# Kernel optimization log

Hardware: AMD Instinct MI355X
Metric: run time of the kernel (lower is better)

## Reference

```python
import jax, jax.numpy as jnp
import numpy as np

B, C, H, W = 8, 32, 512, 512
WS = 8
CQ = C // 4                      # 8
N = (H // WS) * (W // WS)        # 4096 windows
ED = WS * WS * C                 # 2048 embed_dim
EPS = 1e-6


def setup_inputs() -> dict:
    key = jax.random.key(0)
    ks = jax.random.split(key, 16)
    s = 0.02
    return {
        "input_x": jax.random.normal(ks[0], (B, C, H, W), jnp.float32),
        # in_conv: Conv2d(C, C//4, 1)
        "w_in": jax.random.normal(ks[1], (CQ, C), jnp.float32) * s,
        "b_in": jnp.zeros((CQ,), jnp.float32),
        # conv: Conv2d(C, C//4, 1) + LayerNorm(C//4)
        "w_conv": jax.random.normal(ks[2], (CQ, C), jnp.float32) * s,
        "b_conv": jnp.zeros((CQ,), jnp.float32),
        "ln_w": jnp.ones((CQ,), jnp.float32),
        "ln_b": jnp.zeros((CQ,), jnp.float32),
        # out_CA: Conv2d(C//4, C, 1)
        "w_ca": jax.random.normal(ks[3], (C, CQ), jnp.float32) * s,
        "b_ca": jnp.zeros((C,), jnp.float32),
        # out_SA: Conv2d(C//4, 1, 3, pad 1)
        "w_sa": jax.random.normal(ks[4], (1, CQ, 3, 3), jnp.float32) * s,
        "b_sa": jnp.zeros((1,), jnp.float32),
        # out_mask MLP: Linear(ED, ED//2), Linear(ED//2, ED)  (torch weight [out,in])
        "w_m1": jax.random.normal(ks[5], (ED // 2, ED), jnp.float32) * s,
        "b_m1": jnp.zeros((ED // 2,), jnp.float32),
        "w_m2": jax.random.normal(ks[6], (ED, ED // 2), jnp.float32) * s,
        "b_m2": jnp.zeros((ED,), jnp.float32),
    }


def _leaky(x):
    return jax.nn.leaky_relu(x, 0.1)


def _conv1x1(x, w, b):
    # x: [B,Cin,H,W], w: [Cout,Cin]
    return jnp.einsum('bchw,oc->bohw', x, w) + b[None, :, None, None]


def reference(input_x, w_in, b_in, w_conv, b_conv, ln_w, ln_b,
              w_ca, b_ca, w_sa, b_sa, w_m1, b_m1, w_m2, b_m2):
    b_, c_, h_, w_ = input_x.shape
    n_win = (h_ // WS) * (w_ // WS)

    # in_conv branch
    x = _leaky(_conv1x1(input_x, w_in, b_in))          # [B,CQ,H,W]

    # conv branch: 1x1 conv -> channels_first LayerNorm -> leaky
    x_ = _conv1x1(input_x, w_conv, b_conv)             # [B,CQ,H,W]
    u = jnp.mean(x_, axis=1, keepdims=True)
    s = jnp.mean((x_ - u) ** 2, axis=1, keepdims=True)
    x_ = (x_ - u) / jnp.sqrt(s + EPS)
    x_ = _leaky(ln_w[None, :, None, None] * x_ + ln_b[None, :, None, None])

    # channel attention: global avg pool -> 1x1 conv -> sigmoid
    pooled = jnp.mean(x_, axis=(2, 3), keepdims=True)  # [B,CQ,1,1]
    ca = jax.nn.sigmoid(_conv1x1(pooled, w_ca, b_ca))  # [B,C,1,1]

    # spatial attention: 3x3 conv -> sigmoid
    sa = jax.lax.conv_general_dilated(
        x_, w_sa, (1, 1), 'SAME',
        dimension_numbers=('NCHW', 'OIHW', 'NCHW')) + b_sa[None, :, None, None]
    sa = jax.nn.sigmoid(sa)                            # [B,1,H,W]

    # window variance + bottom-k mask
    xm = jnp.mean(x, axis=1)                           # [B,H,W]
    xw = xm.reshape(b_, h_ // WS, WS, w_ // WS, WS)
    xw = xw.transpose(0, 1, 3, 2, 4).reshape(b_, n_win, WS * WS)  # [B,N,64]
    var_x = jnp.var(xw, axis=-1, ddof=1)               # [B,N] (torch unbiased var)
    k_top = n_win // 2
    _, idx = jax.lax.top_k(-var_x, k_top)              # indices of smallest-variance windows
    mask = jnp.ones((b_, n_win), input_x.dtype)
    mask = mask.at[jnp.arange(b_)[:, None], idx].set(0.0)  # vectorized scatter

    # broadcast 0/1 mask across embed dim, then MLP (see notes re: original bug)
    m = jnp.broadcast_to(mask[:, :, None], (b_, n_win, w_m1.shape[1]))
    hdd = _leaky(jnp.einsum('bnd,ed->bne', m, w_m1) + b_m1)
    out_mask = jnp.einsum('bne,fe->bnf', hdd, w_m2) + b_m2  # [B,N,ED]

    return (out_mask, ca, sa)
```

## Files before the change

kernel.cpp:

```cpp
#include <hip/hip_runtime.h>
#include <math.h>

#define B_   8
#define C_   32
#define H_   512
#define W_   512
#define CQ_  8
#define NW_  4096
#define ED_  2048
#define EH_  1024
#define EPS_ 1e-6f

#define TW 64
#define TH 16
#define XLH 18
#define XLW 68

__device__ __forceinline__ float leaky(float x) { return x > 0.f ? x : 0.1f * x; }
__device__ __forceinline__ float sigmoidf_(float x) { return 1.f / (1.f + __expf(-x)); }

__global__ __launch_bounds__(256, 3) void pass_a(
    const float* __restrict__ x,
    const float* __restrict__ w_in, const float* __restrict__ b_in,
    const float* __restrict__ w_conv, const float* __restrict__ b_conv,
    const float* __restrict__ ln_w, const float* __restrict__ ln_b,
    const float* __restrict__ w_sa, const float* __restrict__ b_sa,
    float* __restrict__ sa_out, double* __restrict__ var_out,
    float* __restrict__ pooled_part)
{
    __shared__ float xl[CQ_][XLH][XLW];
    __shared__ float xm_lds[TH][TW];
    __shared__ float red[4][CQ_];

    const int tid = threadIdx.x;
    const int b  = blockIdx.z;
    const int ty = blockIdx.y * TH, tx = blockIdx.x * TW;
    const int px = (tid & 15) * 4, py = tid >> 4;
    const size_t plane = (size_t)H_ * W_;
    const float* xb = x + (size_t)b * C_ * plane;
    const float* p  = xb + (size_t)(ty + py) * W_ + (tx + px);

    int hy = 0, hx = 1;
    if (tid < 66)        { hy = 0;         hx = tid + 1; }
    else if (tid < 132)  { hy = 17;        hx = tid - 65; }
    else if (tid < 148)  { hy = tid - 131; hx = 1; }
    else if (tid < 164)  { hy = tid - 147; hx = 66; }
    const int gy = ty + hy - 1, gx = tx + hx - 2;
    const bool inb = (tid < 164) && (gy >= 0) && (gy < H_) && (gx >= 0) && (gx < W_);
    const float* ph = inb ? (xb + (size_t)gy * W_ + gx) : xb;

    float ycv[CQ_][4], yin[CQ_][4], hacc[CQ_];
#pragma unroll
    for (int q = 0; q < CQ_; ++q) {
        hacc[q] = 0.f;
#pragma unroll
        for (int j = 0; j < 4; ++j) { ycv[q][j] = 0.f; yin[q][j] = 0.f; }
    }

    float4 ib[2][4];
    float  hb[2][4];
#pragma unroll
    for (int k = 0; k < 4; ++k) {
        ib[0][k] = *reinterpret_cast<const float4*>(p + (size_t)k * plane);
        hb[0][k] = ph[(size_t)k * plane];
    }

#pragma unroll
    for (int cb = 0; cb < 8; ++cb) {
        const int cur = cb & 1;
        if (cb < 7) {
#pragma unroll
            for (int k = 0; k < 4; ++k) {
                const int c = (cb + 1) * 4 + k;
                ib[cur ^ 1][k] = *reinterpret_cast<const float4*>(p + (size_t)c * plane);
                hb[cur ^ 1][k] = ph[(size_t)c * plane];
            }
        }
#pragma unroll
        for (int k = 0; k < 4; ++k) {
            const int c = cb * 4 + k;
            const float4 v = ib[cur][k];
            const float hv = hb[cur][k];
#pragma unroll
            for (int q = 0; q < CQ_; ++q) {
                const float wc = w_conv[q * C_ + c];
                const float wi = w_in[q * C_ + c];
                ycv[q][0] = fmaf(wc, v.x, ycv[q][0]);
                ycv[q][1] = fmaf(wc, v.y, ycv[q][1]);
                ycv[q][2] = fmaf(wc, v.z, ycv[q][2]);
                ycv[q][3] = fmaf(wc, v.w, ycv[q][3]);
                yin[q][0] = fmaf(wi, v.x, yin[q][0]);
                yin[q][1] = fmaf(wi, v.y, yin[q][1]);
                yin[q][2] = fmaf(wi, v.z, yin[q][2]);
                yin[q][3] = fmaf(wi, v.w, yin[q][3]);
                hacc[q]   = fmaf(wc, hv, hacc[q]);
            }
        }
    }

#pragma unroll
    for (int q = 0; q < CQ_; ++q) {
        const float bc = b_conv[q];
#pragma unroll
        for (int j = 0; j < 4; ++j) ycv[q][j] += bc;
    }

    float ps[CQ_];
#pragma unroll
    for (int q = 0; q < CQ_; ++q) ps[q] = 0.f;

    float xmv[4];
#pragma unroll
    for (int j = 0; j < 4; ++j) {
        float u = 0.f;
#pragma unroll
        for (int q = 0; q < CQ_; ++q) u += ycv[q][j];
        u *= 0.125f;
        float s = 0.f;
#pragma unroll
        for (int q = 0; q < CQ_; ++q) { const float d = ycv[q][j] - u; s = fmaf(d, d, s); }
        s *= 0.125f;
        const float inv = 1.f / sqrtf(s + EPS_);
        float m = 0.f;
#pragma unroll
        for (int q = 0; q < CQ_; ++q) {
            const float xv = leaky(fmaf(ln_w[q], (ycv[q][j] - u) * inv, ln_b[q]));
            ycv[q][j] = xv;
            ps[q] += xv;
            m += leaky(yin[q][j] + b_in[q]);
        }
        xmv[j] = m * 0.125f;
    }

    *reinterpret_cast<float4*>(&xm_lds[py][px]) = make_float4(xmv[0], xmv[1], xmv[2], xmv[3]);
#pragma unroll
    for (int q = 0; q < CQ_; ++q) {
        *reinterpret_cast<float2*>(&xl[q][py + 1][px + 2]) = make_float2(ycv[q][0], ycv[q][1]);
        *reinterpret_cast<float2*>(&xl[q][py + 1][px + 4]) = make_float2(ycv[q][2], ycv[q][3]);
    }

    const int lane = tid & 63, wave = tid >> 6;
#pragma unroll
    for (int q = 0; q < CQ_; ++q) {
        float s = ps[q];
#pragma unroll
        for (int off = 32; off; off >>= 1) s += __shfl_xor(s, off);
        if (lane == 0) red[wave][q] = s;
    }

    if (tid < 164) {
        float yc[CQ_];
        float u = 0.f;
#pragma unroll
        for (int q = 0; q < CQ_; ++q) { yc[q] = hacc[q] + b_conv[q]; u += yc[q]; }
        u *= 0.125f;
        float s = 0.f;
#pragma unroll
        for (int q = 0; q < CQ_; ++q) { const float d = yc[q] - u; s = fmaf(d, d, s); }
        s *= 0.125f;
        const float inv = 1.f / sqrtf(s + EPS_);
#pragma unroll
        for (int q = 0; q < CQ_; ++q) {
            const float v = leaky(fmaf(ln_w[q], (yc[q] - u) * inv, ln_b[q]));
            xl[q][hy][hx] = inb ? v : 0.f;
        }
    }

    __syncthreads();

    if (tid < CQ_) {
        const float s = red[0][tid] + red[1][tid] + red[2][tid] + red[3][tid];
        const int bid = (blockIdx.z * gridDim.y + blockIdx.y) * gridDim.x + blockIdx.x;
        pooled_part[bid * CQ_ + tid] = s;
    }

    {
        const float bsa = b_sa[0];
        float acc[4] = {bsa, bsa, bsa, bsa};
#pragma unroll
        for (int q = 0; q < CQ_; ++q) {
#pragma unroll
            for (int dy = 0; dy < 3; ++dy) {
                const float* r = &xl[q][py + dy][px];
                const float4 aa = *reinterpret_cast<const float4*>(r);
                const float4 bb = *reinterpret_cast<const float4*>(r + 4);
                const float v[8] = {aa.x, aa.y, aa.z, aa.w, bb.x, bb.y, bb.z, bb.w};
#pragma unroll
                for (int dx = 0; dx < 3; ++dx) {
                    const float w = w_sa[q * 9 + dy * 3 + dx];
#pragma unroll
                    for (int j = 0; j < 4; ++j) acc[j] = fmaf(w, v[j + dx + 1], acc[j]);
                }
            }
        }
        const float4 o = make_float4(sigmoidf_(acc[0]), sigmoidf_(acc[1]),
                                     sigmoidf_(acc[2]), sigmoidf_(acc[3]));
        *reinterpret_cast<float4*>(&sa_out[((size_t)b * H_ + (ty + py)) * W_ + tx + px]) = o;
    }

#pragma unroll
    for (int k = 0; k < 4; ++k) {
        const int wi = wave * 4 + k;
        const int wy = wi >> 3, wx = wi & 7;
        const double dv = (double)xm_lds[wy * 8 + (lane >> 3)][wx * 8 + (lane & 7)];
        double s = dv;
#pragma unroll
        for (int off = 32; off; off >>= 1) s += __shfl_xor(s, off);
        const double mean = s * (1.0 / 64.0);
        const double d = dv - mean;
        double s2 = d * d;
#pragma unroll
        for (int off = 32; off; off >>= 1) s2 += __shfl_xor(s2, off);
        if (lane == 0) {
            const int n = (blockIdx.y * 2 + wy) * 64 + blockIdx.x * 8 + wx;
            var_out[(size_t)b * NW_ + n] = s2 * (1.0 / 63.0);
        }
    }
}

__global__ __launch_bounds__(256) void k2_kernel(
    const double* __restrict__ var, float* __restrict__ maskF,
    const float* __restrict__ w_m1, const float* __restrict__ b_m1,
    float* __restrict__ h1, float* __restrict__ h0,
    const float* __restrict__ pooled_part,
    const float* __restrict__ w_ca, const float* __restrict__ b_ca,
    float* __restrict__ ca_out)
{
    __shared__ double sv[NW_];
    const int bi = blockIdx.x;
    const int tid = threadIdx.x;

    if (bi < 128) {
        const int b = bi >> 4;
        const double* vb = var + (size_t)b * NW_;
        for (int j = tid; j < NW_; j += 256) sv[j] = vb[j];
        __syncthreads();
        const int i = (bi & 15) * 256 + tid;
        const double vi = sv[i];
        int cnt = 0;
#pragma unroll 4
        for (int j = 0; j < NW_; ++j) {
            const double vj = sv[j];
            cnt += (vj < vi) || (vj == vi && j < i);
        }
        maskF[(size_t)b * NW_ + i] = (cnt < NW_ / 2) ? 0.f : 1.f;
    } else if (bi < 384) {
        const int wave = tid >> 6, lane = tid & 63;
        const int e = (bi - 128) * 4 + wave;
        const float* row = w_m1 + (size_t)e * ED_;
        float s = 0.f;
#pragma unroll
        for (int k = 0; k < ED_ / 64; ++k) s += row[lane + 64 * k];
#pragma unroll
        for (int off = 32; off; off >>= 1) s += __shfl_xor(s, off);
        if (lane == 0) {
            h1[e] = leaky(s + b_m1[e]);
            h0[e] = leaky(b_m1[e]);
        }
    } else {
        float* sp = (float*)sv;
        const int bq = tid >> 2, part = tid & 3;
        const int bb = bq >> 3, q = bq & 7;
        float s = 0.f;
        for (int k = part; k < 256; k += 4) s += pooled_part[((size_t)bb * 256 + k) * CQ_ + q];
        sp[tid] = s;
        __syncthreads();
        if (tid < 64)
            sp[256 + tid] = (sp[4 * tid] + sp[4 * tid + 1] + sp[4 * tid + 2] + sp[4 * tid + 3])
                            * (1.f / ((float)H_ * (float)W_));
        __syncthreads();
        const int ob = tid >> 5, o = tid & 31;
        float acc = b_ca[o];
#pragma unroll
        for (int qq = 0; qq < CQ_; ++qq)
            acc = fmaf(w_ca[o * CQ_ + qq], sp[256 + ob * CQ_ + qq], acc);
        ca_out[tid] = sigmoidf_(acc);
    }
}

__global__ __launch_bounds__(256) void o_kernel(const float* __restrict__ w_m2,
                                                const float* __restrict__ b_m2,
                                                const float* __restrict__ h1,
                                                const float* __restrict__ h0,
                                                float* __restrict__ o1, float* __restrict__ o0)
{
    const int wave = threadIdx.x >> 6, lane = threadIdx.x & 63;
    const int f = blockIdx.x * 4 + wave;
    const float* row = w_m2 + (size_t)f * EH_;
    float s1 = 0.f, s0 = 0.f;
#pragma unroll
    for (int k = 0; k < EH_ / 64; ++k) {
        const float w = row[lane + 64 * k];
        s1 = fmaf(w, h1[lane + 64 * k], s1);
        s0 = fmaf(w, h0[lane + 64 * k], s0);
    }
#pragma unroll
    for (int off = 32; off; off >>= 1) {
        s1 += __shfl_xor(s1, off);
        s0 += __shfl_xor(s0, off);
    }
    if (lane == 0) {
        o1[f] = s1 + b_m2[f];
        o0[f] = s0 + b_m2[f];
    }
}

__global__ __launch_bounds__(256) void bcast_kernel(const float* __restrict__ maskF,
                                                    const float* __restrict__ o1,
                                                    const float* __restrict__ o0,
                                                    float* __restrict__ out)
{
    __shared__ float sm[16];
    const int t = threadIdx.x;
    const long row0 = (long)blockIdx.x * 16;
    if (t < 16) sm[t] = maskF[row0 + t];
    const float4 a1 = ((const float4*)o1)[t], b1 = ((const float4*)o1)[t + 256];
    const float4 a0 = ((const float4*)o0)[t], b0 = ((const float4*)o0)[t + 256];
    __syncthreads();
#pragma unroll
    for (int r = 0; r < 16; ++r) {
        float4* dst = (float4*)(out + (size_t)(row0 + r) * ED_);
        const bool m = sm[r] > 0.5f;
        dst[t]       = m ? a1 : a0;
        dst[t + 256] = m ? b1 : b0;
    }
}

extern "C" void kernel_launch(void* const* d_in, const int* in_sizes, int n_in,
                              void* d_out, int out_size, void* d_ws, size_t ws_size,
                              hipStream_t stream)
{
    const float* x    = (const float*)d_in[0];
    const float* w_in = (const float*)d_in[1];
    const float* b_in = (const float*)d_in[2];
    const float* w_cv = (const float*)d_in[3];
    const float* b_cv = (const float*)d_in[4];
    const float* lnw  = (const float*)d_in[5];
    const float* lnb  = (const float*)d_in[6];
    const float* w_ca = (const float*)d_in[7];
    const float* b_ca = (const float*)d_in[8];
    const float* w_sa = (const float*)d_in[9];
    const float* b_sa = (const float*)d_in[10];
    const float* w_m1 = (const float*)d_in[11];
    const float* b_m1 = (const float*)d_in[12];
    const float* w_m2 = (const float*)d_in[13];
    const float* b_m2 = (const float*)d_in[14];

    float* out_mask = (float*)d_out;
    float* ca_out   = out_mask + (size_t)B_ * NW_ * ED_;
    float* sa_out   = ca_out + (size_t)B_ * C_;

    char* ws = (char*)d_ws;
    double* var       = (double*)ws;
    float*  maskF     = (float*)(ws + (size_t)B_ * NW_ * 8);
    float*  pooled_pp = maskF + (size_t)B_ * NW_;
    float*  h1 = pooled_pp + 2048 * CQ_;
    float*  h0 = h1 + EH_;
    float*  o1 = h0 + EH_;
    float*  o0 = o1 + ED_;

    pass_a<<<dim3(W_ / TW, H_ / TH, B_), 256, 0, stream>>>(
        x, w_in, b_in, w_cv, b_cv, lnw, lnb, w_sa, b_sa, sa_out, var, pooled_pp);
    k2_kernel<<<385, 256, 0, stream>>>(var, maskF, w_m1, b_m1, h1, h0,
                                       pooled_pp, w_ca, b_ca, ca_out);
    o_kernel<<<ED_ / 4, 256, 0, stream>>>(w_m2, b_m2, h1, h0, o1, o0);
    bcast_kernel<<<B_ * NW_ / 16, 256, 0, stream>>>(maskF, o1, o0, out_mask);
}
```

Before: 331.8 us.

## Split spatial-attention conv into separate kernel and stage input via global_load_lds

The first pass no longer recomputes the LayerNorm branch on a 1-pixel halo for the 3x3 conv. Instead it writes the normalized CQ-channel map into the (later overwritten) out_mask buffer, and a new sa_kernel does the 3x3 conv plus sigmoid from that intermediate. The input channel loads are moved to asynchronous global-to-LDS copies, double-buffered and synchronized with barriers, and the occupancy hint is raised from 3 to 4. This removes the halo loads and redundant halo compute in exchange for an extra 64MB write and read of the intermediate and an additional kernel launch.

```diff
diff --git a/kernel.cpp b/kernel.cpp
--- a/kernel.cpp
+++ b/kernel.cpp
@@ -13,22 +13,23 @@
 
 #define TW 64
 #define TH 16
-#define XLH 18
-#define XLW 68
+
+#define AS1 __attribute__((address_space(1)))
+#define AS3 __attribute__((address_space(3)))
 
 __device__ __forceinline__ float leaky(float x) { return x > 0.f ? x : 0.1f * x; }
 __device__ __forceinline__ float sigmoidf_(float x) { return 1.f / (1.f + __expf(-x)); }
 
-__global__ __launch_bounds__(256, 3) void pass_a(
+__global__ __launch_bounds__(256, 4) void pass_a(
     const float* __restrict__ x,
     const float* __restrict__ w_in, const float* __restrict__ b_in,
     const float* __restrict__ w_conv, const float* __restrict__ b_conv,
     const float* __restrict__ ln_w, const float* __restrict__ ln_b,
-    const float* __restrict__ w_sa, const float* __restrict__ b_sa,
-    float* __restrict__ sa_out, double* __restrict__ var_out,
+    float* __restrict__ xq_out,
+    double* __restrict__ var_out,
     float* __restrict__ pooled_part)
 {
-    __shared__ float xl[CQ_][XLH][XLW];
+    __shared__ float stage[2][4][TH][TW];
     __shared__ float xm_lds[TH][TW];
     __shared__ float red[4][CQ_];
 
@@ -36,51 +37,49 @@
     const int b  = blockIdx.z;
     const int ty = blockIdx.y * TH, tx = blockIdx.x * TW;
     const int px = (tid & 15) * 4, py = tid >> 4;
+    const int lane = tid & 63, wv = tid >> 6;
     const size_t plane = (size_t)H_ * W_;
     const float* xb = x + (size_t)b * C_ * plane;
-    const float* p  = xb + (size_t)(ty + py) * W_ + (tx + px);
-
-    int hy = 0, hx = 1;
-    if (tid < 66)        { hy = 0;         hx = tid + 1; }
-    else if (tid < 132)  { hy = 17;        hx = tid - 65; }
-    else if (tid < 148)  { hy = tid - 131; hx = 1; }
-    else if (tid < 164)  { hy = tid - 147; hx = 66; }
-    const int gy = ty + hy - 1, gx = tx + hx - 2;
-    const bool inb = (tid < 164) && (gy >= 0) && (gy < H_) && (gx >= 0) && (gx < W_);
-    const float* ph = inb ? (xb + (size_t)gy * W_ + gx) : xb;
-
-    float ycv[CQ_][4], yin[CQ_][4], hacc[CQ_];
-#pragma unroll
-    for (int q = 0; q < CQ_; ++q) {
-        hacc[q] = 0.f;
+
+    const float* gsrc[4];
+#pragma unroll
+    for (int i = 0; i < 4; ++i) {
+        const int j = i * 64 + lane;
+        const int r = j >> 4, c4 = j & 15;
+        gsrc[i] = xb + (size_t)wv * plane + (size_t)(ty + r) * W_ + tx + c4 * 4;
+    }
+
+#define STAGE(bufidx, cb)                                                     \
+    {                                                                         \
+        _Pragma("unroll")                                                     \
+        for (int i_ = 0; i_ < 4; ++i_) {                                      \
+            __builtin_amdgcn_global_load_lds(                                 \
+                (const AS1 unsigned int*)(gsrc[i_] + (size_t)(cb) * 4 * plane),\
+                (AS3 unsigned int*)(&stage[bufidx][wv][0][0] + i_ * 256),     \
+                16, 0, 0);                                                    \
+        }                                                                     \
+    }
+
+    float ycv[CQ_][4], yin[CQ_][4];
+#pragma unroll
+    for (int q = 0; q < CQ_; ++q)
 #pragma unroll
         for (int j = 0; j < 4; ++j) { ycv[q][j] = 0.f; yin[q][j] = 0.f; }
-    }
-
-    float4 ib[2][4];
-    float  hb[2][4];
-#pragma unroll
-    for (int k = 0; k < 4; ++k) {
-        ib[0][k] = *reinterpret_cast<const float4*>(p + (size_t)k * plane);
-        hb[0][k] = ph[(size_t)k * plane];
-    }
-
+
+    STAGE(0, 0);
 #pragma unroll
     for (int cb = 0; cb < 8; ++cb) {
-        const int cur = cb & 1;
         if (cb < 7) {
-#pragma unroll
-            for (int k = 0; k < 4; ++k) {
-                const int c = (cb + 1) * 4 + k;
-                ib[cur ^ 1][k] = *reinterpret_cast<const float4*>(p + (size_t)c * plane);
-                hb[cur ^ 1][k] = ph[(size_t)c * plane];
-            }
-        }
+            STAGE((cb + 1) & 1, cb + 1);
+            asm volatile("s_waitcnt vmcnt(4)" ::: "memory");
+        } else {
+            asm volatile("s_waitcnt vmcnt(0)" ::: "memory");
+        }
+        asm volatile("s_barrier" ::: "memory");
 #pragma unroll
         for (int k = 0; k < 4; ++k) {
             const int c = cb * 4 + k;
-            const float4 v = ib[cur][k];
-            const float hv = hb[cur][k];
+            const float4 v = *reinterpret_cast<const float4*>(&stage[cb & 1][k][py][px]);
 #pragma unroll
             for (int q = 0; q < CQ_; ++q) {
                 const float wc = w_conv[q * C_ + c];
@@ -93,10 +92,11 @@
                 yin[q][1] = fmaf(wi, v.y, yin[q][1]);
                 yin[q][2] = fmaf(wi, v.z, yin[q][2]);
                 yin[q][3] = fmaf(wi, v.w, yin[q][3]);
-                hacc[q]   = fmaf(wc, hv, hacc[q]);
             }
         }
-    }
+        asm volatile("s_barrier" ::: "memory");
+    }
+#undef STAGE
 
 #pragma unroll
     for (int q = 0; q < CQ_; ++q) {
@@ -132,38 +132,21 @@
         xmv[j] = m * 0.125f;
     }
 
+#pragma unroll
+    for (int q = 0; q < CQ_; ++q) {
+        *reinterpret_cast<float4*>(
+            &xq_out[(((size_t)b * CQ_ + q) * H_ + (ty + py)) * W_ + tx + px]) =
+            make_float4(ycv[q][0], ycv[q][1], ycv[q][2], ycv[q][3]);
+    }
+
     *reinterpret_cast<float4*>(&xm_lds[py][px]) = make_float4(xmv[0], xmv[1], xmv[2], xmv[3]);
-#pragma unroll
-    for (int q = 0; q < CQ_; ++q) {
-        *reinterpret_cast<float2*>(&xl[q][py + 1][px + 2]) = make_float2(ycv[q][0], ycv[q][1]);
-        *reinterpret_cast<float2*>(&xl[q][py + 1][px + 4]) = make_float2(ycv[q][2], ycv[q][3]);
-    }
-
-    const int lane = tid & 63, wave = tid >> 6;
+
 #pragma unroll
     for (int q = 0; q < CQ_; ++q) {
         float s = ps[q];
 #pragma unroll
         for (int off = 32; off; off >>= 1) s += __shfl_xor(s, off);
-        if (lane == 0) red[wave][q] = s;
-    }
-
-    if (tid < 164) {
-        float yc[CQ_];
-        float u = 0.f;
-#pragma unroll
-        for (int q = 0; q < CQ_; ++q) { yc[q] = hacc[q] + b_conv[q]; u += yc[q]; }
-        u *= 0.125f;
-        float s = 0.f;
-#pragma unroll
-        for (int q = 0; q < CQ_; ++q) { const float d = yc[q] - u; s = fmaf(d, d, s); }
-        s *= 0.125f;
-        const float inv = 1.f / sqrtf(s + EPS_);
-#pragma unroll
-        for (int q = 0; q < CQ_; ++q) {
-            const float v = leaky(fmaf(ln_w[q], (yc[q] - u) * inv, ln_b[q]));
-            xl[q][hy][hx] = inb ? v : 0.f;
-        }
+        if (lane == 0) red[wv][q] = s;
     }
 
     __syncthreads();
@@ -174,33 +157,9 @@
         pooled_part[bid * CQ_ + tid] = s;
     }
 
-    {
-        const float bsa = b_sa[0];
-        float acc[4] = {bsa, bsa, bsa, bsa};
-#pragma unroll
-        for (int q = 0; q < CQ_; ++q) {
-#pragma unroll
-            for (int dy = 0; dy < 3; ++dy) {
-                const float* r = &xl[q][py + dy][px];
-                const float4 aa = *reinterpret_cast<const float4*>(r);
-                const float4 bb = *reinterpret_cast<const float4*>(r + 4);
-                const float v[8] = {aa.x, aa.y, aa.z, aa.w, bb.x, bb.y, bb.z, bb.w};
-#pragma unroll
-                for (int dx = 0; dx < 3; ++dx) {
-                    const float w = w_sa[q * 9 + dy * 3 + dx];
-#pragma unroll
-                    for (int j = 0; j < 4; ++j) acc[j] = fmaf(w, v[j + dx + 1], acc[j]);
-                }
-            }
-        }
-        const float4 o = make_float4(sigmoidf_(acc[0]), sigmoidf_(acc[1]),
-                                     sigmoidf_(acc[2]), sigmoidf_(acc[3]));
-        *reinterpret_cast<float4*>(&sa_out[((size_t)b * H_ + (ty + py)) * W_ + tx + px]) = o;
-    }
-
 #pragma unroll
     for (int k = 0; k < 4; ++k) {
-        const int wi = wave * 4 + k;
+        const int wi = wv * 4 + k;
         const int wy = wi >> 3, wx = wi & 7;
         const double dv = (double)xm_lds[wy * 8 + (lane >> 3)][wx * 8 + (lane & 7)];
         double s = dv;
@@ -216,6 +175,56 @@
             var_out[(size_t)b * NW_ + n] = s2 * (1.0 / 63.0);
         }
     }
+}
+
+__global__ __launch_bounds__(256) void sa_kernel(
+    const float* __restrict__ xq,
+    const float* __restrict__ w_sa, const float* __restrict__ b_sa,
+    float* __restrict__ sa_out)
+{
+    __shared__ float xl[CQ_][18][72];
+    const int tid = threadIdx.x;
+    const int b = blockIdx.z;
+    const int ty = blockIdx.y * TH, tx = blockIdx.x * TW;
+
+    for (int idx = tid; idx < CQ_ * 18 * 18; idx += 256) {
+        const int ch = idx / 324;
+        const int rem = idx % 324;
+        const int r = rem / 18, c4 = rem % 18;
+        const int gy = ty + r - 1;
+        const int gxf = tx + c4 * 4 - 4;
+        float4 v = make_float4(0.f, 0.f, 0.f, 0.f);
+        if (gy >= 0 && gy < H_ && gxf >= 0 && gxf < W_)
+            v = *reinterpret_cast<const float4*>(
+                    &xq[(((size_t)b * CQ_ + ch) * H_ + gy) * W_ + gxf]);
+        *reinterpret_cast<float4*>(&xl[ch][r][c4 * 4]) = v;
+    }
+    __syncthreads();
+
+    const int px = (tid & 15) * 4, py = tid >> 4;
+    const float bsa = b_sa[0];
+    float acc[4] = {bsa, bsa, bsa, bsa};
+#pragma unroll
+    for (int q = 0; q < CQ_; ++q) {
+#pragma unroll
+        for (int dy = 0; dy < 3; ++dy) {
+            const float* r = &xl[q][py + dy][px];
+            const float4 aa = *reinterpret_cast<const float4*>(r);
+            const float4 bb = *reinterpret_cast<const float4*>(r + 4);
+            const float4 cc = *reinterpret_cast<const float4*>(r + 8);
+            const float a[12] = {aa.x, aa.y, aa.z, aa.w, bb.x, bb.y, bb.z, bb.w,
+                                 cc.x, cc.y, cc.z, cc.w};
+#pragma unroll
+            for (int dx = 0; dx < 3; ++dx) {
+                const float w = w_sa[q * 9 + dy * 3 + dx];
+#pragma unroll
+                for (int j = 0; j < 4; ++j) acc[j] = fmaf(w, a[j + 3 + dx], acc[j]);
+            }
+        }
+    }
+    const float4 o = make_float4(sigmoidf_(acc[0]), sigmoidf_(acc[1]),
+                                 sigmoidf_(acc[2]), sigmoidf_(acc[3]));
+    *reinterpret_cast<float4*>(&sa_out[((size_t)b * H_ + (ty + py)) * W_ + tx + px]) = o;
 }
 
 __global__ __launch_bounds__(256) void k2_kernel(
@@ -350,6 +359,8 @@
     float* ca_out   = out_mask + (size_t)B_ * NW_ * ED_;
     float* sa_out   = ca_out + (size_t)B_ * C_;
 
+    float* xq = out_mask;
+
     char* ws = (char*)d_ws;
     double* var       = (double*)ws;
     float*  maskF     = (float*)(ws + (size_t)B_ * NW_ * 8);
@@ -360,7 +371,8 @@
     float*  o0 = o1 + ED_;
 
     pass_a<<<dim3(W_ / TW, H_ / TH, B_), 256, 0, stream>>>(
-        x, w_in, b_in, w_cv, b_cv, lnw, lnb, w_sa, b_sa, sa_out, var, pooled_pp);
+        x, w_in, b_in, w_cv, b_cv, lnw, lnb, xq, var, pooled_pp);
+    sa_kernel<<<dim3(W_ / TW, H_ / TH, B_), 256, 0, stream>>>(xq, w_sa, b_sa, sa_out);
     k2_kernel<<<385, 256, 0, stream>>>(var, maskF, w_m1, b_m1, h1, h0,
                                        pooled_pp, w_ca, b_ca, ca_out);
     o_kernel<<<ED_ / 4, 256, 0, stream>>>(w_m2, b_m2, h1, h0, o1, o0);
```

After: 333.4 us. No clear change (+0.5%).
